# Optimization experiments

Measured on AMD Instinct MI355X. Metric: run time of the kernel, lower is better.

The kernel has to match this reference:

```python
import jax, jax.numpy as jnp
import numpy as np

BETA = 0.5      # conf.beta (undefined global in original repo)
ALPHA = 0.2     # LeakyReLU negative slope (init arg alpha)
N, E, FIN, FOUT = 50000, 1_600_000, 128, 64


def setup_inputs() -> dict:
    key = jax.random.key(0)
    k1, k2, k3, k4, k5 = jax.random.split(key, 5)
    inp = jax.random.normal(k1, (N, FIN), dtype=jnp.float32)
    edge = jax.random.randint(k2, (2, E), 0, N)                      # [2,E] (src,dst), = adj.nonzero().t()
    M_vals = jax.random.uniform(k3, (E,), dtype=jnp.float32)          # M gathered at edges
    # xavier_normal with gain 1.414, matching torch init
    W = jax.random.normal(k4, (FIN, FOUT), dtype=jnp.float32) * (1.414 * np.sqrt(2.0 / (FIN + FOUT)))
    a = jax.random.normal(k5, (2 * FOUT,), dtype=jnp.float32) * (1.414 * np.sqrt(2.0 / (1 + 2 * FOUT)))
    return {"input": inp, "M_vals": M_vals, "W": W, "a": a, "edge": edge}


def reference(input, M_vals, W, a, edge):
    n, f = input.shape[0], W.shape[1]
    src, dst = edge[0], edge[1]
    h = input @ W                                   # [N, F]
    # M = beta*M + (1-beta)*adj; at edges adj == 1
    bias = M_vals * BETA + (1.0 - BETA)             # [E]
    # a . cat(h_src, bias*h_dst) == (h@a[:F])[src] + bias * (h@a[F:])[dst]
    s1 = h @ a[:f]                                  # [N]
    s2 = h @ a[f:]                                  # [N]
    edge_e = jnp.exp(jax.nn.leaky_relu(s1[src] + bias * s2[dst], negative_slope=ALPHA))  # [E]
    # special_spmm(edge, e, [N,N], ones) -> per-row sum of edge weights
    e_rowsum = jax.ops.segment_sum(edge_e, src, num_segments=n)       # [N]
    # special_spmm(edge, e, [N,N], h) -> weighted aggregation of dst features into src rows
    h_prime = jax.ops.segment_sum(edge_e[:, None] * h[dst], src, num_segments=n)  # [N, F]
    h_prime = h_prime / e_rowsum[:, None]
    return jax.nn.elu(h_prime)                      # concat=True
```

## Files before the change

### kernel.cpp

```cpp
#include <hip/hip_runtime.h>
#include <hip/hip_bf16.h>

#define NN   50000
#define EE   1600000
#define FIN  128
#define FOUT 64
#define BETA  0.5f
#define ALPHA 0.2f
#define SBW    64
#define SBSH   6
#define NB     782
#define RCAP   2500
#define PGRID  400
#define PCHUNK 4000
#define CAPB   2504
#define XS     136

typedef __attribute__((ext_vector_type(8))) short short8;
typedef __attribute__((ext_vector_type(8))) unsigned short ushort8v;
typedef __attribute__((ext_vector_type(4))) float float4v;

__device__ __forceinline__ float load_any(const void* p, long i, int isf32) {
    if (isf32) return ((const float*)p)[i];
    unsigned int b = ((unsigned int)(((const unsigned short*)p)[i])) << 16;
    return __uint_as_float(b);
}

__device__ __forceinline__ unsigned short f32_to_bf16_rne(float f) {
    unsigned int b = __float_as_uint(f);
    return (unsigned short)((b + 0x7FFF + ((b >> 16) & 1)) >> 16);
}

__device__ __forceinline__ float bf16_to_f32(unsigned short u) {
    return __uint_as_float(((unsigned int)u) << 16);
}

__global__ __launch_bounds__(256) void detwt_kernel(
    const void* __restrict__ W, const void* __restrict__ Mv,
    unsigned short* __restrict__ Wt, int* __restrict__ flags,
    int* __restrict__ bcur)
{
    __shared__ int vote;
    const int tid = threadIdx.x;
    if (tid == 0) vote = 0;
    __syncthreads();

    int m = 0;
    const float vw = bf16_to_f32(((const unsigned short*)W)[tid * 16]);
    if (isnan(vw) || fabsf(vw) > 1e4f) m |= 1;
    if (blockIdx.x == 0) {
        const long half = (long)EE >> 1;
        const long pos = 2 * (((long)tid * (half / 256)) % half);
        const float vm = bf16_to_f32(((const unsigned short*)Mv)[pos]);
        if (isnan(vm) || fabsf(vm) > 1e4f) m |= 2;
    }
    if (m) atomicOr(&vote, m);
    __syncthreads();

    const int fW = vote & 1;
    if (blockIdx.x == 0) {
        if (tid == 0) flags[1] = (vote >> 1) & 1;
        for (int i = tid; i < NB; i += 256) bcur[i] = 0;
    }
    const int i = blockIdx.x * 256 + tid;
    const int k = i >> 6, n = i & 63;
    Wt[n * FIN + k] = f32_to_bf16_rne(load_any(W, i, fW));
}

__global__ __launch_bounds__(256) void mfma_gemm_kernel(
    const void* __restrict__ inp,
    const unsigned short* __restrict__ Wt,
    const void* __restrict__ a,
    unsigned short* __restrict__ h,
    float* __restrict__ s1,
    float* __restrict__ s2,
    int* __restrict__ flags)
{
    __shared__ unsigned short Xs[16 * XS];
    __shared__ float part1[4][16];
    __shared__ float part2[4][16];
    __shared__ int vote;

    const int tid  = threadIdx.x;
    const int wave = tid >> 6;
    const int lane = tid & 63;
    const int quad = lane >> 4;
    const int col  = lane & 15;
    const int rb   = blockIdx.x * 16;

    if (tid == 0) vote = 0;
    __syncthreads();

    {
        int m = 0;
        const float vi = bf16_to_f32(((const unsigned short*)inp)[(long)rb * FIN + tid * 8]);
        if (isnan(vi) || fabsf(vi) > 1e4f) m |= 1;
        if (tid < 128) {
            const float va = bf16_to_f32(((const unsigned short*)a)[tid]);
            if (isnan(va) || fabsf(va) > 1e4f) m |= 2;
        }
        if (m) atomicOr(&vote, m);
    }
    __syncthreads();
    const int fI = vote & 1, fA = (vote >> 1) & 1;
    if (blockIdx.x == 0 && tid == 0) flags[0] = fI;

    {
        const int r = tid >> 4, k8 = (tid & 15) * 8;
        if (!fI) {
            const unsigned short* src = (const unsigned short*)inp + (long)(rb + r) * FIN + k8;
            *(ushort8v*)&Xs[r * XS + k8] = *(const ushort8v*)src;
        } else {
            const float* src = (const float*)inp + (long)(rb + r) * FIN + k8;
            ushort8v v;
            #pragma unroll
            for (int j = 0; j < 8; ++j) v[j] = f32_to_bf16_rne(src[j]);
            *(ushort8v*)&Xs[r * XS + k8] = v;
        }
    }
    __syncthreads();

    const int nb = wave * 16;
    float4v acc = { 0.f, 0.f, 0.f, 0.f };
    #pragma unroll
    for (int k0 = 0; k0 < FIN; k0 += 32) {
        const short8 af = *(const short8*)&Xs[col * XS + k0 + quad * 8];
        const short8 bf = *(const short8*)&Wt[(long)(nb + col) * FIN + k0 + quad * 8];
        acc = __builtin_amdgcn_mfma_f32_16x16x32_bf16(af, bf, acc, 0, 0, 0);
    }

    #pragma unroll
    for (int r = 0; r < 4; ++r)
        h[(long)(rb + quad * 4 + r) * FOUT + nb + col] = f32_to_bf16_rne(acc[r]);

    const float a1 = load_any(a, nb + col, fA);
    const float a2 = load_any(a, 64 + nb + col, fA);
    #pragma unroll
    for (int r = 0; r < 4; ++r) {
        float v1 = acc[r] * a1;
        float v2 = acc[r] * a2;
        #pragma unroll
        for (int o = 1; o < 16; o <<= 1) {
            v1 += __shfl_xor(v1, o, 64);
            v2 += __shfl_xor(v2, o, 64);
        }
        if (col == 0) {
            part1[wave][quad * 4 + r] = v1;
            part2[wave][quad * 4 + r] = v2;
        }
    }
    __syncthreads();
    if (tid < 16) {
        s1[rb + tid] = part1[0][tid] + part1[1][tid] + part1[2][tid] + part1[3][tid];
        s2[rb + tid] = part2[0][tid] + part2[1][tid] + part2[2][tid] + part2[3][tid];
    }
}

__global__ __launch_bounds__(1024) void partition_kernel(
    const int* __restrict__ edge,
    const void* __restrict__ Mv,
    const int* __restrict__ flags,
    const float* __restrict__ s1,
    const float* __restrict__ s2,
    int* __restrict__ bcur,
    unsigned long long* __restrict__ recs)
{
    __shared__ int lcnt[NB];
    __shared__ int lbase[NB];
    const int tid = threadIdx.x;
    const int fM = flags[1];
    const int e0 = blockIdx.x * PCHUNK;

    if (tid < NB) lcnt[tid] = 0;
    __syncthreads();

    int srcs[4], dsts[4];
    float mvs[4];
    #pragma unroll
    for (int k = 0; k < 4; ++k) {
        const int e = e0 + tid + 1024 * k;
        const bool ok = (tid + 1024 * k) < PCHUNK;
        srcs[k] = ok ? edge[e] : -1;
        dsts[k] = ok ? edge[EE + e] : 0;
        mvs[k]  = ok ? load_any(Mv, e, fM) : 0.f;
    }
    #pragma unroll
    for (int k = 0; k < 4; ++k)
        if (srcs[k] >= 0) atomicAdd(&lcnt[srcs[k] >> SBSH], 1);
    __syncthreads();

    if (tid < NB) {
        const int c = lcnt[tid];
        const int o = c ? atomicAdd(&bcur[tid], c) : 0;
        lbase[tid] = tid * RCAP + o;
        lcnt[tid] = 0;
    }
    __syncthreads();

    float ss1[4], ss2[4];
    #pragma unroll
    for (int k = 0; k < 4; ++k) {
        ss1[k] = (srcs[k] >= 0) ? s1[srcs[k]] : 0.f;
        ss2[k] = (srcs[k] >= 0) ? s2[dsts[k]] : 0.f;
    }
    #pragma unroll
    for (int k = 0; k < 4; ++k) {
        if (srcs[k] < 0) continue;
        const float bias = mvs[k] * BETA + (1.f - BETA);
        const float x  = ss1[k] + bias * ss2[k];
        const float lr = x > 0.f ? x : ALPHA * x;
        const float ee = __expf(lr);
        const int b = srcs[k] >> SBSH;
        const int r = atomicAdd(&lcnt[b], 1);
        const int pos = lbase[b] + r;
        if (pos < (b + 1) * RCAP)
            recs[pos] = ((unsigned long long)(unsigned)srcs[k] << 32)
                      | ((unsigned long long)(unsigned)dsts[k] << 16)
                      | (unsigned long long)f32_to_bf16_rne(ee);
    }
}

__global__ __launch_bounds__(512) void csr_spmm_kernel(
    const int* __restrict__ bcur,
    const unsigned long long* __restrict__ recs,
    const unsigned short* __restrict__ h,
    const int* __restrict__ flags,
    void* __restrict__ out)
{
    __shared__ unsigned long long lrec[CAPB];
    __shared__ unsigned int lpair[CAPB];
    __shared__ int cnt[SBW];
    __shared__ int off[SBW];
    const int b    = blockIdx.x;
    const int tid  = threadIdx.x;
    const int rb   = b * SBW;
    const int beg  = b * RCAP;

    int n = bcur[b]; if (n > RCAP) n = RCAP;

    if (tid < SBW) cnt[tid] = 0;
    __syncthreads();

    for (int j = tid; j < n; j += 512) {
        const unsigned long long rec = recs[beg + j];
        const int r = (int)(rec >> 32) - rb;
        const int rank = atomicAdd(&cnt[r], 1);
        lrec[j] = ((unsigned long long)(unsigned)(r | (rank << 8)) << 32)
                | (unsigned long long)(unsigned)(rec & 0xFFFFFFFFu);
    }
    __syncthreads();

    if (tid < SBW) {
        const int c = cnt[tid];
        int x = c;
        #pragma unroll
        for (int o = 1; o < SBW; o <<= 1) {
            int y = __shfl_up(x, o, 64);
            if (tid >= o) x += y;
        }
        off[tid] = x - c;
    }
    __syncthreads();

    for (int j = tid; j < n; j += 512) {
        const unsigned long long rec = lrec[j];
        const unsigned int hi = (unsigned int)(rec >> 32);
        lpair[off[hi & 63u] + (hi >> 8)] = (unsigned int)(rec & 0xFFFFFFFFu);
    }
    __syncthreads();

    const int wv   = tid >> 6;
    const int lane = tid & 63;
    const int gr   = lane >> 3;
    const int sl   = lane & 7;
    const int rr   = wv * 8 + gr;
    const int row  = rb + rr;
    const int fOut = flags[0];

    const int jb = off[rr];
    const int je = jb + cnt[rr];

    float acc0 = 0.f, acc1 = 0.f, acc2 = 0.f, acc3 = 0.f;
    float acc4 = 0.f, acc5 = 0.f, acc6 = 0.f, acc7 = 0.f;
    float rsum = 0.f;
    int j = jb;
    for (; j + 3 < je; j += 4) {
        unsigned int u[4];
        #pragma unroll
        for (int kk = 0; kk < 4; ++kk) u[kk] = lpair[j + kk];
        ushort8v hv[4];
        #pragma unroll
        for (int kk = 0; kk < 4; ++kk)
            hv[kk] = *(const ushort8v*)&h[(long)(u[kk] >> 16) * FOUT + 8 * sl];
        #pragma unroll
        for (int kk = 0; kk < 4; ++kk) {
            const float v = bf16_to_f32((unsigned short)(u[kk] & 0xFFFFu));
            rsum += v;
            acc0 = fmaf(v, bf16_to_f32(hv[kk][0]), acc0);
            acc1 = fmaf(v, bf16_to_f32(hv[kk][1]), acc1);
            acc2 = fmaf(v, bf16_to_f32(hv[kk][2]), acc2);
            acc3 = fmaf(v, bf16_to_f32(hv[kk][3]), acc3);
            acc4 = fmaf(v, bf16_to_f32(hv[kk][4]), acc4);
            acc5 = fmaf(v, bf16_to_f32(hv[kk][5]), acc5);
            acc6 = fmaf(v, bf16_to_f32(hv[kk][6]), acc6);
            acc7 = fmaf(v, bf16_to_f32(hv[kk][7]), acc7);
        }
    }
    for (; j < je; ++j) {
        const unsigned int u = lpair[j];
        const ushort8v hv = *(const ushort8v*)&h[(long)(u >> 16) * FOUT + 8 * sl];
        const float v = bf16_to_f32((unsigned short)(u & 0xFFFFu));
        rsum += v;
        acc0 = fmaf(v, bf16_to_f32(hv[0]), acc0);
        acc1 = fmaf(v, bf16_to_f32(hv[1]), acc1);
        acc2 = fmaf(v, bf16_to_f32(hv[2]), acc2);
        acc3 = fmaf(v, bf16_to_f32(hv[3]), acc3);
        acc4 = fmaf(v, bf16_to_f32(hv[4]), acc4);
        acc5 = fmaf(v, bf16_to_f32(hv[5]), acc5);
        acc6 = fmaf(v, bf16_to_f32(hv[6]), acc6);
        acc7 = fmaf(v, bf16_to_f32(hv[7]), acc7);
    }

    if (row < NN && je > jb) {
        const float inv = 1.f / rsum;
        float q0 = acc0 * inv, q1 = acc1 * inv, q2 = acc2 * inv, q3 = acc3 * inv;
        float q4 = acc4 * inv, q5 = acc5 * inv, q6 = acc6 * inv, q7 = acc7 * inv;
        q0 = q0 > 0.f ? q0 : (__expf(q0) - 1.f);
        q1 = q1 > 0.f ? q1 : (__expf(q1) - 1.f);
        q2 = q2 > 0.f ? q2 : (__expf(q2) - 1.f);
        q3 = q3 > 0.f ? q3 : (__expf(q3) - 1.f);
        q4 = q4 > 0.f ? q4 : (__expf(q4) - 1.f);
        q5 = q5 > 0.f ? q5 : (__expf(q5) - 1.f);
        q6 = q6 > 0.f ? q6 : (__expf(q6) - 1.f);
        q7 = q7 > 0.f ? q7 : (__expf(q7) - 1.f);
        if (fOut) {
            float4* o = (float4*)((float*)out + (long)row * FOUT + 8 * sl);
            o[0] = make_float4(q0, q1, q2, q3);
            o[1] = make_float4(q4, q5, q6, q7);
        } else {
            ushort8v ov;
            ov[0] = f32_to_bf16_rne(q0); ov[1] = f32_to_bf16_rne(q1);
            ov[2] = f32_to_bf16_rne(q2); ov[3] = f32_to_bf16_rne(q3);
            ov[4] = f32_to_bf16_rne(q4); ov[5] = f32_to_bf16_rne(q5);
            ov[6] = f32_to_bf16_rne(q6); ov[7] = f32_to_bf16_rne(q7);
            *(ushort8v*)((unsigned short*)out + (long)row * FOUT + 8 * sl) = ov;
        }
    } else if (row < NN) {
        if (fOut) {
            float4* o = (float4*)((float*)out + (long)row * FOUT + 8 * sl);
            o[0] = make_float4(0.f, 0.f, 0.f, 0.f);
            o[1] = make_float4(0.f, 0.f, 0.f, 0.f);
        } else {
            ushort8v ov = { 0, 0, 0, 0, 0, 0, 0, 0 };
            *(ushort8v*)((unsigned short*)out + (long)row * FOUT + 8 * sl) = ov;
        }
    }
}

extern "C" void kernel_launch(void* const* d_in, const int* in_sizes, int n_in,
                              void* d_out, int out_size, void* d_ws, size_t ws_size,
                              hipStream_t stream) {
    const void* inp  = d_in[0];
    const void* Mv   = d_in[1];
    const void* W    = d_in[2];
    const void* a    = d_in[3];
    const int*  edge = (const int*)d_in[4];

    char* p = (char*)d_ws;
    int*                flags  = (int*)p;            p += 256;
    unsigned short*     Wt     = (unsigned short*)p; p += ((size_t)FOUT * FIN * 2 + 255) / 256 * 256;
    unsigned short*     h      = (unsigned short*)p; p += ((size_t)NN * FOUT * 2 + 255) / 256 * 256;
    float*              s1     = (float*)p;          p += ((size_t)NN * 4 + 255) / 256 * 256;
    float*              s2     = (float*)p;          p += ((size_t)NN * 4 + 255) / 256 * 256;
    int*                bcur   = (int*)p;            p += ((size_t)NB * 4 + 255) / 256 * 256;
    unsigned long long* recs   = (unsigned long long*)p;

    detwt_kernel<<<32, 256, 0, stream>>>(W, Mv, Wt, flags, bcur);
    mfma_gemm_kernel<<<NN / 16, 256, 0, stream>>>(inp, Wt, a, h, s1, s2, flags);
    partition_kernel<<<PGRID, 1024, 0, stream>>>(edge, Mv, flags, s1, s2, bcur, recs);
    csr_spmm_kernel<<<NB, 512, 0, stream>>>(bcur, recs, h, flags, d_out);
}
```

Before: 155.3 us.

## Replace block-bucketed partition with per-row fixed-capacity slots via global atomics

Drops the two-level bucket partition (per-block shared-memory counts, then an in-shared sort into CSR order) in favour of direct per-row slots. Each edge atomically increments a global per-row counter and writes a packed 32-bit (dst, bf16 weight) record into a fixed 80-slot region for its source row. The SpMM kernel then reads each row's records straight from global memory, with no shared-memory staging, sort or prefix scan. This saves the shared-memory reorganisation and shrinks records from 8 to 4 bytes. In exchange it adds 1.6M global atomics over 50K counters, and any row with more than 80 edges is silently truncated.

```diff
diff --git a/kernel.cpp b/kernel.cpp
--- a/kernel.cpp
+++ b/kernel.cpp
@@ -7,14 +7,9 @@
 #define FOUT 64
 #define BETA  0.5f
 #define ALPHA 0.2f
-#define SBW    64
-#define SBSH   6
-#define NB     782
-#define RCAP   2500
-#define PGRID  400
-#define PCHUNK 4000
-#define CAPB   2504
-#define XS     136
+#define RCAPR 80
+#define DGRID 196
+#define XS    136
 
 typedef __attribute__((ext_vector_type(8))) short short8;
 typedef __attribute__((ext_vector_type(8))) unsigned short ushort8v;
@@ -38,33 +33,37 @@
 __global__ __launch_bounds__(256) void detwt_kernel(
     const void* __restrict__ W, const void* __restrict__ Mv,
     unsigned short* __restrict__ Wt, int* __restrict__ flags,
-    int* __restrict__ bcur)
+    int* __restrict__ rowcnt)
 {
     __shared__ int vote;
     const int tid = threadIdx.x;
     if (tid == 0) vote = 0;
     __syncthreads();
 
-    int m = 0;
-    const float vw = bf16_to_f32(((const unsigned short*)W)[tid * 16]);
-    if (isnan(vw) || fabsf(vw) > 1e4f) m |= 1;
-    if (blockIdx.x == 0) {
-        const long half = (long)EE >> 1;
-        const long pos = 2 * (((long)tid * (half / 256)) % half);
-        const float vm = bf16_to_f32(((const unsigned short*)Mv)[pos]);
-        if (isnan(vm) || fabsf(vm) > 1e4f) m |= 2;
-    }
-    if (m) atomicOr(&vote, m);
-    __syncthreads();
-
-    const int fW = vote & 1;
-    if (blockIdx.x == 0) {
-        if (tid == 0) flags[1] = (vote >> 1) & 1;
-        for (int i = tid; i < NB; i += 256) bcur[i] = 0;
-    }
-    const int i = blockIdx.x * 256 + tid;
-    const int k = i >> 6, n = i & 63;
-    Wt[n * FIN + k] = f32_to_bf16_rne(load_any(W, i, fW));
+    {
+        const int i = blockIdx.x * 256 + tid;
+        if (i < NN) rowcnt[i] = 0;
+    }
+
+    if (blockIdx.x < 32) {
+        int m = 0;
+        const float vw = bf16_to_f32(((const unsigned short*)W)[tid * 16]);
+        if (isnan(vw) || fabsf(vw) > 1e4f) m |= 1;
+        if (blockIdx.x == 0) {
+            const long half = (long)EE >> 1;
+            const long pos = 2 * (((long)tid * (half / 256)) % half);
+            const float vm = bf16_to_f32(((const unsigned short*)Mv)[pos]);
+            if (isnan(vm) || fabsf(vm) > 1e4f) m |= 2;
+        }
+        if (m) atomicOr(&vote, m);
+        __syncthreads();
+
+        const int fW = vote & 1;
+        if (blockIdx.x == 0 && tid == 0) flags[1] = (vote >> 1) & 1;
+        const int i = blockIdx.x * 256 + tid;
+        const int k = i >> 6, n = i & 63;
+        Wt[n * FIN + k] = f32_to_bf16_rne(load_any(W, i, fW));
+    }
 }
 
 __global__ __launch_bounds__(256) void mfma_gemm_kernel(
@@ -156,138 +155,75 @@
     }
 }
 
-__global__ __launch_bounds__(1024) void partition_kernel(
+__global__ __launch_bounds__(256) void edge_kernel(
     const int* __restrict__ edge,
     const void* __restrict__ Mv,
     const int* __restrict__ flags,
     const float* __restrict__ s1,
     const float* __restrict__ s2,
-    int* __restrict__ bcur,
-    unsigned long long* __restrict__ recs)
+    int* __restrict__ rowcnt,
+    unsigned int* __restrict__ rrec)
 {
-    __shared__ int lcnt[NB];
-    __shared__ int lbase[NB];
-    const int tid = threadIdx.x;
+    const long e0 = ((long)blockIdx.x * 256 + threadIdx.x) * 4;
+    if (e0 >= EE) return;
     const int fM = flags[1];
-    const int e0 = blockIdx.x * PCHUNK;
-
-    if (tid < NB) lcnt[tid] = 0;
-    __syncthreads();
-
-    int srcs[4], dsts[4];
-    float mvs[4];
+
+    const int4 s4 = *(const int4*)&edge[e0];
+    const int4 d4 = *(const int4*)&edge[EE + e0];
+    const int ss[4] = { s4.x, s4.y, s4.z, s4.w };
+    const int dd[4] = { d4.x, d4.y, d4.z, d4.w };
+
+    float mv[4];
+    if (fM) {
+        const float4 m4 = *(const float4*)((const float*)Mv + e0);
+        mv[0] = m4.x; mv[1] = m4.y; mv[2] = m4.z; mv[3] = m4.w;
+    } else {
+        const ushort4 m4 = *(const ushort4*)((const unsigned short*)Mv + e0);
+        mv[0] = bf16_to_f32(m4.x); mv[1] = bf16_to_f32(m4.y);
+        mv[2] = bf16_to_f32(m4.z); mv[3] = bf16_to_f32(m4.w);
+    }
+
+    float v1[4], v2[4];
+    #pragma unroll
+    for (int k = 0; k < 4; ++k) { v1[k] = s1[ss[k]]; v2[k] = s2[dd[k]]; }
+
     #pragma unroll
     for (int k = 0; k < 4; ++k) {
-        const int e = e0 + tid + 1024 * k;
-        const bool ok = (tid + 1024 * k) < PCHUNK;
-        srcs[k] = ok ? edge[e] : -1;
-        dsts[k] = ok ? edge[EE + e] : 0;
-        mvs[k]  = ok ? load_any(Mv, e, fM) : 0.f;
-    }
-    #pragma unroll
-    for (int k = 0; k < 4; ++k)
-        if (srcs[k] >= 0) atomicAdd(&lcnt[srcs[k] >> SBSH], 1);
-    __syncthreads();
-
-    if (tid < NB) {
-        const int c = lcnt[tid];
-        const int o = c ? atomicAdd(&bcur[tid], c) : 0;
-        lbase[tid] = tid * RCAP + o;
-        lcnt[tid] = 0;
-    }
-    __syncthreads();
-
-    float ss1[4], ss2[4];
-    #pragma unroll
-    for (int k = 0; k < 4; ++k) {
-        ss1[k] = (srcs[k] >= 0) ? s1[srcs[k]] : 0.f;
-        ss2[k] = (srcs[k] >= 0) ? s2[dsts[k]] : 0.f;
-    }
-    #pragma unroll
-    for (int k = 0; k < 4; ++k) {
-        if (srcs[k] < 0) continue;
-        const float bias = mvs[k] * BETA + (1.f - BETA);
-        const float x  = ss1[k] + bias * ss2[k];
+        const float bias = mv[k] * BETA + (1.f - BETA);
+        const float x  = v1[k] + bias * v2[k];
         const float lr = x > 0.f ? x : ALPHA * x;
         const float ee = __expf(lr);
-        const int b = srcs[k] >> SBSH;
-        const int r = atomicAdd(&lcnt[b], 1);
-        const int pos = lbase[b] + r;
-        if (pos < (b + 1) * RCAP)
-            recs[pos] = ((unsigned long long)(unsigned)srcs[k] << 32)
-                      | ((unsigned long long)(unsigned)dsts[k] << 16)
-                      | (unsigned long long)f32_to_bf16_rne(ee);
-    }
-}
-
-__global__ __launch_bounds__(512) void csr_spmm_kernel(
-    const int* __restrict__ bcur,
-    const unsigned long long* __restrict__ recs,
+        const int pos = atomicAdd(&rowcnt[ss[k]], 1);
+        if (pos < RCAPR)
+            rrec[(long)ss[k] * RCAPR + pos] =
+                ((unsigned int)dd[k] << 16) | f32_to_bf16_rne(ee);
+    }
+}
+
+__global__ __launch_bounds__(256) void spmm_kernel(
+    const int* __restrict__ rowcnt,
+    const unsigned int* __restrict__ rrec,
     const unsigned short* __restrict__ h,
     const int* __restrict__ flags,
     void* __restrict__ out)
 {
-    __shared__ unsigned long long lrec[CAPB];
-    __shared__ unsigned int lpair[CAPB];
-    __shared__ int cnt[SBW];
-    __shared__ int off[SBW];
-    const int b    = blockIdx.x;
-    const int tid  = threadIdx.x;
-    const int rb   = b * SBW;
-    const int beg  = b * RCAP;
-
-    int n = bcur[b]; if (n > RCAP) n = RCAP;
-
-    if (tid < SBW) cnt[tid] = 0;
-    __syncthreads();
-
-    for (int j = tid; j < n; j += 512) {
-        const unsigned long long rec = recs[beg + j];
-        const int r = (int)(rec >> 32) - rb;
-        const int rank = atomicAdd(&cnt[r], 1);
-        lrec[j] = ((unsigned long long)(unsigned)(r | (rank << 8)) << 32)
-                | (unsigned long long)(unsigned)(rec & 0xFFFFFFFFu);
-    }
-    __syncthreads();
-
-    if (tid < SBW) {
-        const int c = cnt[tid];
-        int x = c;
-        #pragma unroll
-        for (int o = 1; o < SBW; o <<= 1) {
-            int y = __shfl_up(x, o, 64);
-            if (tid >= o) x += y;
-        }
-        off[tid] = x - c;
-    }
-    __syncthreads();
-
-    for (int j = tid; j < n; j += 512) {
-        const unsigned long long rec = lrec[j];
-        const unsigned int hi = (unsigned int)(rec >> 32);
-        lpair[off[hi & 63u] + (hi >> 8)] = (unsigned int)(rec & 0xFFFFFFFFu);
-    }
-    __syncthreads();
-
-    const int wv   = tid >> 6;
-    const int lane = tid & 63;
-    const int gr   = lane >> 3;
-    const int sl   = lane & 7;
-    const int rr   = wv * 8 + gr;
-    const int row  = rb + rr;
+    const int tid = threadIdx.x;
+    const int grp = tid >> 3;
+    const int sl  = tid & 7;
+    const int row = blockIdx.x * 32 + grp;
+    if (row >= NN) return;
+
+    int cnt = rowcnt[row]; if (cnt > RCAPR) cnt = RCAPR;
+    const unsigned int* rbase = rrec + (long)row * RCAPR;
     const int fOut = flags[0];
-
-    const int jb = off[rr];
-    const int je = jb + cnt[rr];
 
     float acc0 = 0.f, acc1 = 0.f, acc2 = 0.f, acc3 = 0.f;
     float acc4 = 0.f, acc5 = 0.f, acc6 = 0.f, acc7 = 0.f;
     float rsum = 0.f;
-    int j = jb;
-    for (; j + 3 < je; j += 4) {
-        unsigned int u[4];
-        #pragma unroll
-        for (int kk = 0; kk < 4; ++kk) u[kk] = lpair[j + kk];
+    int j = 0;
+    for (; j + 3 < cnt; j += 4) {
+        const uint4 uu = *(const uint4*)&rbase[j];
+        const unsigned int u[4] = { uu.x, uu.y, uu.z, uu.w };
         ushort8v hv[4];
         #pragma unroll
         for (int kk = 0; kk < 4; ++kk)
@@ -306,8 +242,8 @@
             acc7 = fmaf(v, bf16_to_f32(hv[kk][7]), acc7);
         }
     }
-    for (; j < je; ++j) {
-        const unsigned int u = lpair[j];
+    for (; j < cnt; ++j) {
+        const unsigned int u = rbase[j];
         const ushort8v hv = *(const ushort8v*)&h[(long)(u >> 16) * FOUT + 8 * sl];
         const float v = bf16_to_f32((unsigned short)(u & 0xFFFFu));
         rsum += v;
@@ -321,7 +257,7 @@
         acc7 = fmaf(v, bf16_to_f32(hv[7]), acc7);
     }
 
-    if (row < NN && je > jb) {
+    if (cnt > 0) {
         const float inv = 1.f / rsum;
         float q0 = acc0 * inv, q1 = acc1 * inv, q2 = acc2 * inv, q3 = acc3 * inv;
         float q4 = acc4 * inv, q5 = acc5 * inv, q6 = acc6 * inv, q7 = acc7 * inv;
@@ -345,7 +281,7 @@
             ov[6] = f32_to_bf16_rne(q6); ov[7] = f32_to_bf16_rne(q7);
             *(ushort8v*)((unsigned short*)out + (long)row * FOUT + 8 * sl) = ov;
         }
-    } else if (row < NN) {
+    } else {
         if (fOut) {
             float4* o = (float4*)((float*)out + (long)row * FOUT + 8 * sl);
             o[0] = make_float4(0.f, 0.f, 0.f, 0.f);
@@ -367,16 +303,16 @@
     const int*  edge = (const int*)d_in[4];
 
     char* p = (char*)d_ws;
-    int*                flags  = (int*)p;            p += 256;
-    unsigned short*     Wt     = (unsigned short*)p; p += ((size_t)FOUT * FIN * 2 + 255) / 256 * 256;
-    unsigned short*     h      = (unsigned short*)p; p += ((size_t)NN * FOUT * 2 + 255) / 256 * 256;
-    float*              s1     = (float*)p;          p += ((size_t)NN * 4 + 255) / 256 * 256;
-    float*              s2     = (float*)p;          p += ((size_t)NN * 4 + 255) / 256 * 256;
-    int*                bcur   = (int*)p;            p += ((size_t)NB * 4 + 255) / 256 * 256;
-    unsigned long long* recs   = (unsigned long long*)p;
-
-    detwt_kernel<<<32, 256, 0, stream>>>(W, Mv, Wt, flags, bcur);
+    int*            flags  = (int*)p;            p += 256;
+    unsigned short* Wt     = (unsigned short*)p; p += ((size_t)FOUT * FIN * 2 + 255) / 256 * 256;
+    unsigned short* h      = (unsigned short*)p; p += ((size_t)NN * FOUT * 2 + 255) / 256 * 256;
+    float*          s1     = (float*)p;          p += ((size_t)NN * 4 + 255) / 256 * 256;
+    float*          s2     = (float*)p;          p += ((size_t)NN * 4 + 255) / 256 * 256;
+    int*            rowcnt = (int*)p;            p += ((size_t)NN * 4 + 255) / 256 * 256;
+    unsigned int*   rrec   = (unsigned int*)p;
+
+    detwt_kernel<<<DGRID, 256, 0, stream>>>(W, Mv, Wt, flags, rowcnt);
     mfma_gemm_kernel<<<NN / 16, 256, 0, stream>>>(inp, Wt, a, h, s1, s2, flags);
-    partition_kernel<<<PGRID, 1024, 0, stream>>>(edge, Mv, flags, s1, s2, bcur, recs);
-    csr_spmm_kernel<<<NB, 512, 0, stream>>>(bcur, recs, h, flags, d_out);
-}
+    edge_kernel<<<(EE / 4 + 255) / 256, 256, 0, stream>>>(edge, Mv, flags, s1, s2, rowcnt, rrec);
+    spmm_kernel<<<(NN + 31) / 32, 256, 0, stream>>>(rowcnt, rrec, h, flags, d_out);
+}
```

Measured after the change: 231.7 us. 1.49x slower.
